# Performance work log

Measured on AMD Instinct MI355X. Metric: run time of the kernel, lower is better.

The kernel has to match this reference:

```python
import jax, jax.numpy as jnp
import numpy as np

N_NODES = 100000
N_EDGES = 1600000
IN_CH = 128          # 127 node features + 1 node_attr
HIDDEN = 2           # hidd_FV_size
OUT_CH = 128
ATTR = 6


def setup_inputs() -> dict:
    key = jax.random.key(0)
    ks = jax.random.split(key, 8)
    x = jax.random.normal(ks[0], (N_NODES, IN_CH - 1), dtype=jnp.float32)
    node_attr = jax.random.normal(ks[1], (N_NODES, 1), dtype=jnp.float32)
    edge_index = jax.random.randint(ks[2], (2, N_EDGES), 0, N_NODES, dtype=jnp.int64)
    edge_attr = jax.random.normal(ks[3], (N_EDGES, ATTR), dtype=jnp.float32)
    # lin_in: Linear(ATTR, HIDDEN * IN_CH); lin_out: Linear(HIDDEN * IN_CH, OUT_CH)
    W_in = jax.random.normal(ks[4], (ATTR, HIDDEN * IN_CH), dtype=jnp.float32) / np.sqrt(ATTR)
    b_in = jax.random.normal(ks[5], (HIDDEN * IN_CH,), dtype=jnp.float32) * 0.01
    W_out = jax.random.normal(ks[6], (HIDDEN * IN_CH, OUT_CH), dtype=jnp.float32) / np.sqrt(HIDDEN * IN_CH)
    b_out = jax.random.normal(ks[7], (OUT_CH,), dtype=jnp.float32) * 0.01
    return {"x": x, "node_attr": node_attr, "edge_index": edge_index,
            "edge_attr": edge_attr, "W_in": W_in, "b_in": b_in,
            "W_out": W_out, "b_out": b_out}


def reference(x, node_attr, edge_index, edge_attr, W_in, b_in, W_out, b_out):
    # forward: x = cat(x, node_attr) -> propagate(aggr='add') -> update
    xc = jnp.concatenate([x, node_attr], axis=1)                # [N, IN_CH]
    src, dst = edge_index[0], edge_index[1]                     # PyG: message from x_j=src, aggregated at dst
    x_j = xc[src]                                               # [E, IN_CH] gather
    # message: scaling = relu(lin_in(edge_attr)); result = scaling.reshape(E,C,H) * x_j[...,None]
    scaling = jax.nn.relu(edge_attr @ W_in + b_in)              # [E, C*H]
    msg = (scaling.reshape(-1, IN_CH, HIDDEN) * x_j[:, :, None]).reshape(-1, IN_CH * HIDDEN)
    # aggregate: scatter-add over destination nodes
    aggr = jax.ops.segment_sum(msg, dst, num_segments=N_NODES)  # [N, C*H]
    # update: lin_out -> tanh (dropout p=0 / eval mode)
    return jnp.tanh(aggr @ W_out + b_out)                       # [N, OUT_CH]
```

## Files before the change

### kernel.cpp

```cpp
#include <hip/hip_runtime.h>


#define ATTR 6
#define SCAN_CHUNK 1024


__global__ __launch_bounds__(256) void concat_kernel(
    const float* __restrict__ x, const float* __restrict__ na,
    float* __restrict__ xc, int N)
{
  const int gid = blockIdx.x * 256 + threadIdx.x;
  const int row = gid >> 5;
  const int c4 = (gid & 31) * 4;
  if (row >= N) return;
  const float* xr = x + (size_t)row * 127;
  float4 v;
  v.x = xr[c4];
  v.y = xr[c4 + 1];
  v.z = xr[c4 + 2];
  v.w = (c4 == 124) ? na[row] : xr[c4 + 3];
  *(float4*)(xc + (size_t)row * 128 + c4) = v;
}


__global__ __launch_bounds__(256) void hist_kernel(
    const int* __restrict__ ei, int* __restrict__ counts, int E)
{
  int e = blockIdx.x * 256 + threadIdx.x;
  if (e < E) atomicAdd(&counts[ei[E + e]], 1);
}

__global__ __launch_bounds__(256) void scan1_kernel(
    const int* __restrict__ counts, int* __restrict__ offsets,
    int* __restrict__ bsum, int N)
{
  __shared__ int sdata[256];
  const int t = threadIdx.x;
  const int base = blockIdx.x * SCAN_CHUNK + t * 4;
  int c[4]; int s = 0;
#pragma unroll
  for (int j = 0; j < 4; ++j) { int i = base + j; c[j] = (i < N) ? counts[i] : 0; s += c[j]; }
  sdata[t] = s;
  __syncthreads();
  for (int d = 1; d < 256; d <<= 1) {
    int tv = (t >= d) ? sdata[t - d] : 0;
    __syncthreads();
    sdata[t] += tv;
    __syncthreads();
  }
  int excl = sdata[t] - s;
#pragma unroll
  for (int j = 0; j < 4; ++j) { int i = base + j; if (i < N) offsets[i] = excl; excl += c[j]; }
  if (t == 255) bsum[blockIdx.x] = sdata[255];
}

__global__ __launch_bounds__(256) void scan2_kernel(int* __restrict__ bsum, int nb)
{
  __shared__ int sdata[256];
  const int t = threadIdx.x;
  int v = (t < nb) ? bsum[t] : 0;
  int orig = v;
  sdata[t] = v;
  __syncthreads();
  for (int d = 1; d < 256; d <<= 1) {
    int tv = (t >= d) ? sdata[t - d] : 0;
    __syncthreads();
    sdata[t] += tv;
    __syncthreads();
  }
  if (t < nb) bsum[t] = sdata[t] - orig;
}

__global__ __launch_bounds__(256) void scan3_kernel(
    int* __restrict__ offsets, int* __restrict__ cursors,
    const int* __restrict__ bsum, int N, int E)
{
  const int base = blockIdx.x * SCAN_CHUNK + threadIdx.x * 4;
  const int add = bsum[blockIdx.x];
#pragma unroll
  for (int j = 0; j < 4; ++j) {
    int i = base + j;
    if (i < N) { int v = offsets[i] + add; offsets[i] = v; cursors[i] = v; }
  }
  if (blockIdx.x == 0 && threadIdx.x == 0) offsets[N] = E;
}

__global__ __launch_bounds__(256) void scatter_payload_kernel(
    const int* __restrict__ ei, const float* __restrict__ ea,
    int* __restrict__ cursors,
    int* __restrict__ srcs, float* __restrict__ eas, int E)
{
  int e = blockIdx.x * 256 + threadIdx.x;
  if (e < E) {
    const int dst = ei[E + e];
    const int slot = atomicAdd(&cursors[dst], 1);
    srcs[slot] = ei[e];
    const float2 a0 = *(const float2*)(ea + (size_t)e * ATTR + 0);
    const float2 a1 = *(const float2*)(ea + (size_t)e * ATTR + 2);
    const float2 a2 = *(const float2*)(ea + (size_t)e * ATTR + 4);
    float* ep = eas + (size_t)slot * ATTR;
    *(float2*)(ep + 0) = a0;
    *(float2*)(ep + 2) = a1;
    *(float2*)(ep + 4) = a2;
  }
}

__global__ __launch_bounds__(256) void scatter_kernel(
    const int* __restrict__ ei, int* __restrict__ cursors,
    int* __restrict__ perm, int* __restrict__ srcs, int E)
{
  int e = blockIdx.x * 256 + threadIdx.x;
  if (e < E) {
    int dst = ei[E + e];
    int slot = atomicAdd(&cursors[dst], 1);
    perm[slot] = e;
    srcs[slot] = ei[e];
  }
}


__global__ __launch_bounds__(256) void aggregate8_kernel(
    const float* __restrict__ xc,
    const float* __restrict__ W_in, const float* __restrict__ b_in,
    const int* __restrict__ offsets, const int* __restrict__ srcs,
    const float* __restrict__ eas,
    float* __restrict__ aggr, int N)
{
  const int L = threadIdx.x & 63;
  const int n = __builtin_amdgcn_readfirstlane(blockIdx.x * 4 + (threadIdx.x >> 6));
  if (n >= N) return;

  float2 wlo[ATTR], whi[ATTR];
#pragma unroll
  for (int a = 0; a < ATTR; ++a) {
    wlo[a] = *(const float2*)(W_in + a * 256 + 2 * L);
    whi[a] = *(const float2*)(W_in + a * 256 + 128 + 2 * L);
  }
  const float2 blo = *(const float2*)(b_in + 2 * L);
  const float2 bhi = *(const float2*)(b_in + 128 + 2 * L);

  float alo0 = 0.f, alo1 = 0.f, ahi0 = 0.f, ahi1 = 0.f;
  const int beg = offsets[n], end = offsets[n + 1];

  for (int i0 = beg; i0 < end; i0 += 8) {
    const int cnt = end - i0;
    int s8[8];
#pragma unroll
    for (int j = 0; j < 8; ++j) {
      const int idx = i0 + ((j < cnt) ? j : cnt - 1);
      s8[j] = srcs[idx];
    }
    float eav[8][ATTR];
#pragma unroll
    for (int j = 0; j < 8; ++j) {
      const int idx = i0 + ((j < cnt) ? j : cnt - 1);
#pragma unroll
      for (int a = 0; a < ATTR; ++a) eav[j][a] = eas[(size_t)idx * ATTR + a];
    }

    float xlo[8], xhi[8];
#pragma unroll
    for (int j = 0; j < 8; ++j) {
      const float* xr = xc + (size_t)s8[j] * 128;
      xlo[j] = xr[L];
      xhi[j] = xr[64 + L];
    }
#pragma unroll
    for (int j = 0; j < 8; ++j)
      if (j >= cnt) { xlo[j] = 0.f; xhi[j] = 0.f; }

#pragma unroll
    for (int j = 0; j < 8; ++j) {
      float sl0 = blo.x, sl1 = blo.y, sh0 = bhi.x, sh1 = bhi.y;
#pragma unroll
      for (int a = 0; a < ATTR; ++a) {
        sl0 = fmaf(eav[j][a], wlo[a].x, sl0);
        sl1 = fmaf(eav[j][a], wlo[a].y, sl1);
        sh0 = fmaf(eav[j][a], whi[a].x, sh0);
        sh1 = fmaf(eav[j][a], whi[a].y, sh1);
      }
      sl0 = fmaxf(sl0, 0.f); sl1 = fmaxf(sl1, 0.f);
      sh0 = fmaxf(sh0, 0.f); sh1 = fmaxf(sh1, 0.f);
      alo0 = fmaf(sl0, xlo[j], alo0);
      alo1 = fmaf(sl1, xlo[j], alo1);
      ahi0 = fmaf(sh0, xhi[j], ahi0);
      ahi1 = fmaf(sh1, xhi[j], ahi1);
    }
  }

  *(float2*)(aggr + (size_t)n * 256 + 2 * L)       = make_float2(alo0, alo1);
  *(float2*)(aggr + (size_t)n * 256 + 128 + 2 * L) = make_float2(ahi0, ahi1);
}


__global__ __launch_bounds__(256) void aggregate4_kernel(
    const float* __restrict__ x, const float* __restrict__ node_attr,
    const int* __restrict__ ei, const float* __restrict__ ea,
    const float* __restrict__ W_in, const float* __restrict__ b_in,
    const int* __restrict__ offsets, const int* __restrict__ perm,
    const int* __restrict__ srcs,
    float* __restrict__ aggr, int N)
{
  const int L = threadIdx.x & 63;
  const int n = __builtin_amdgcn_readfirstlane(blockIdx.x * 4 + (threadIdx.x >> 6));
  if (n >= N) return;

  float2 wlo[ATTR], whi[ATTR];
#pragma unroll
  for (int a = 0; a < ATTR; ++a) {
    wlo[a] = *(const float2*)(W_in + a * 256 + 2 * L);
    whi[a] = *(const float2*)(W_in + a * 256 + 128 + 2 * L);
  }
  const float2 blo = *(const float2*)(b_in + 2 * L);
  const float2 bhi = *(const float2*)(b_in + 128 + 2 * L);

  float alo0 = 0.f, alo1 = 0.f, ahi0 = 0.f, ahi1 = 0.f;
  const int beg = offsets[n], end = offsets[n + 1];

  for (int i0 = beg; i0 < end; i0 += 4) {
    const int cnt = end - i0;
    int e4[4], s4[4];
#pragma unroll
    for (int j = 0; j < 4; ++j) {
      const int idx = i0 + ((j < cnt) ? j : cnt - 1);
      e4[j] = perm[idx];
      s4[j] = srcs[idx];
    }

    float eav[4][ATTR];
#pragma unroll
    for (int j = 0; j < 4; ++j)
#pragma unroll
      for (int a = 0; a < ATTR; ++a) eav[j][a] = ea[(size_t)e4[j] * ATTR + a];

    float xlo[4], xhi[4];
#pragma unroll
    for (int j = 0; j < 4; ++j) {
      const float* xr = x + (size_t)s4[j] * 127;
      xlo[j] = xr[L];
      xhi[j] = (L == 63) ? node_attr[s4[j]] : xr[64 + L];
    }
#pragma unroll
    for (int j = 0; j < 4; ++j)
      if (j >= cnt) { xlo[j] = 0.f; xhi[j] = 0.f; }

#pragma unroll
    for (int j = 0; j < 4; ++j) {
      float sl0 = blo.x, sl1 = blo.y, sh0 = bhi.x, sh1 = bhi.y;
#pragma unroll
      for (int a = 0; a < ATTR; ++a) {
        sl0 = fmaf(eav[j][a], wlo[a].x, sl0);
        sl1 = fmaf(eav[j][a], wlo[a].y, sl1);
        sh0 = fmaf(eav[j][a], whi[a].x, sh0);
        sh1 = fmaf(eav[j][a], whi[a].y, sh1);
      }
      sl0 = fmaxf(sl0, 0.f); sl1 = fmaxf(sl1, 0.f);
      sh0 = fmaxf(sh0, 0.f); sh1 = fmaxf(sh1, 0.f);
      alo0 = fmaf(sl0, xlo[j], alo0);
      alo1 = fmaf(sl1, xlo[j], alo1);
      ahi0 = fmaf(sh0, xhi[j], ahi0);
      ahi1 = fmaf(sh1, xhi[j], ahi1);
    }
  }

  *(float2*)(aggr + (size_t)n * 256 + 2 * L)       = make_float2(alo0, alo1);
  *(float2*)(aggr + (size_t)n * 256 + 128 + 2 * L) = make_float2(ahi0, ahi1);
}


__global__ __launch_bounds__(256) void edge_kernel(
    const float* __restrict__ x, const float* __restrict__ node_attr,
    const int* __restrict__ ei, const float* __restrict__ ea,
    const float* __restrict__ W_in, const float* __restrict__ b_in,
    float* __restrict__ aggr, int E, int N, int epw)
{
  const int lane = threadIdx.x & 63;
  const int wave = blockIdx.x * (blockDim.x >> 6) + (threadIdx.x >> 6);
  const int k0 = lane << 2;
  const int c0 = lane << 1;

  float w[ATTR][4];
#pragma unroll
  for (int a = 0; a < ATTR; ++a) {
    const float4 t = *(const float4*)(W_in + a * 256 + k0);
    w[a][0] = t.x; w[a][1] = t.y; w[a][2] = t.z; w[a][3] = t.w;
  }
  const float4 bt = *(const float4*)(b_in + k0);

  const long e0 = (long)wave * epw;
  for (int i = 0; i < epw; ++i) {
    const long e = e0 + i;
    if (e >= E) return;
    const int src = ei[e];
    const int dst = ei[E + e];

    float eav[ATTR];
#pragma unroll
    for (int a = 0; a < ATTR; ++a) eav[a] = ea[(size_t)e * ATTR + a];

    float s0 = bt.x, s1 = bt.y, s2 = bt.z, s3 = bt.w;
#pragma unroll
    for (int a = 0; a < ATTR; ++a) {
      s0 = fmaf(eav[a], w[a][0], s0);
      s1 = fmaf(eav[a], w[a][1], s1);
      s2 = fmaf(eav[a], w[a][2], s2);
      s3 = fmaf(eav[a], w[a][3], s3);
    }
    s0 = fmaxf(s0, 0.f); s1 = fmaxf(s1, 0.f);
    s2 = fmaxf(s2, 0.f); s3 = fmaxf(s3, 0.f);

    const float* xr = x + (size_t)src * 127;
    const float x0 = xr[c0];
    const float x1 = (lane == 63) ? node_attr[src] : xr[c0 + 1];

    float* ap = aggr + (size_t)dst * 256 + k0;
    atomicAdd(ap + 0, s0 * x0);
    atomicAdd(ap + 1, s1 * x0);
    atomicAdd(ap + 2, s2 * x1);
    atomicAdd(ap + 3, s3 * x1);
  }
}


__global__ __launch_bounds__(256) void node_kernel2(
    const float* __restrict__ aggr, const float* __restrict__ W_out,
    const float* __restrict__ b_out, float* __restrict__ out, int N)
{
  __shared__ float Wl[64 * 128];
  __shared__ float Al[64][68];
  const int t = threadIdx.x;
  const int o4 = (t & 31) * 4;
  const int ng = t >> 5;
  const int nbase = blockIdx.x * 64;

  float acc[8][4];
#pragma unroll
  for (int j = 0; j < 8; ++j)
#pragma unroll
    for (int q = 0; q < 4; ++q) acc[j][q] = 0.f;

  for (int kc = 0; kc < 4; ++kc) {
    __syncthreads();
    const float4* wsrc = (const float4*)(W_out + kc * 64 * 128);
    float4* wdst = (float4*)Wl;
#pragma unroll
    for (int i = 0; i < 8; ++i) wdst[t + 256 * i] = wsrc[t + 256 * i];
    {
      const int r = t >> 2, q = t & 3;
      int row = nbase + r; if (row >= N) row = N - 1;
      const float4* asrc = (const float4*)(aggr + (size_t)row * 256 + kc * 64 + q * 16);
      float4 v0 = asrc[0], v1 = asrc[1], v2 = asrc[2], v3 = asrc[3];
      float4* adst = (float4*)&Al[r][q * 16];
      adst[0] = v0; adst[1] = v1; adst[2] = v2; adst[3] = v3;
    }
    __syncthreads();

    for (int k = 0; k < 64; k += 4) {
      float4 a4[8];
#pragma unroll
      for (int j = 0; j < 8; ++j) a4[j] = *(const float4*)&Al[ng * 8 + j][k];
#pragma unroll
      for (int kk = 0; kk < 4; ++kk) {
        const float4 w4 = *(const float4*)&Wl[(k + kk) * 128 + o4];
#pragma unroll
        for (int j = 0; j < 8; ++j) {
          const float av = (&a4[j].x)[kk];
          acc[j][0] = fmaf(av, w4.x, acc[j][0]);
          acc[j][1] = fmaf(av, w4.y, acc[j][1]);
          acc[j][2] = fmaf(av, w4.z, acc[j][2]);
          acc[j][3] = fmaf(av, w4.w, acc[j][3]);
        }
      }
    }
  }

  const float4 b4 = *(const float4*)(b_out + o4);
#pragma unroll
  for (int j = 0; j < 8; ++j) {
    const int n = nbase + ng * 8 + j;
    if (n < N) {
      float4 r;
      r.x = tanhf(acc[j][0] + b4.x);
      r.y = tanhf(acc[j][1] + b4.y);
      r.z = tanhf(acc[j][2] + b4.z);
      r.w = tanhf(acc[j][3] + b4.w);
      *(float4*)(out + (size_t)n * 128 + o4) = r;
    }
  }
}


extern "C" void kernel_launch(void* const* d_in, const int* in_sizes, int n_in,
                              void* d_out, int out_size, void* d_ws, size_t ws_size,
                              hipStream_t stream) {
  const float* x         = (const float*)d_in[0];
  const float* node_attr = (const float*)d_in[1];
  const int*   ei        = (const int*)d_in[2];
  const float* ea        = (const float*)d_in[3];
  const float* W_in      = (const float*)d_in[4];
  const float* b_in      = (const float*)d_in[5];
  const float* W_out     = (const float*)d_in[6];
  const float* b_out     = (const float*)d_in[7];
  float* out = (float*)d_out;

  const int N = in_sizes[0] / 127;
  const int E = in_sizes[2] / 2;

  auto align16 = [](size_t v) { return (v + 15) & ~(size_t)15; };
  const size_t szCounts  = align16((size_t)N * 4);
  const size_t szOffsets = align16(((size_t)N + 1) * 4);
  const size_t szCursors = align16((size_t)N * 4);
  const size_t szBsum    = 1024;
  const size_t szPerm    = align16((size_t)E * 4);
  const size_t szSrcs    = align16((size_t)E * 4);
  const size_t szEas     = align16((size_t)E * ATTR * 4);
  const size_t szXc      = align16((size_t)N * 128 * 4);
  const size_t szAggr    = (size_t)N * 256 * 4;

  const size_t needA = szCounts + szOffsets + szCursors + szBsum +
                       szSrcs + szEas + szXc + szAggr;
  const size_t needB = szCounts + szOffsets + szCursors + szBsum +
                       szPerm + szSrcs + szAggr;

  const int nodeBlocks = (N + 63) / 64;
  const int eb = (E + 255) / 256;
  const int nb = (N + SCAN_CHUNK - 1) / SCAN_CHUNK;

  if (ws_size >= needA) {
    char* p = (char*)d_ws;
    int* counts   = (int*)p;     p += szCounts;
    int* offsets  = (int*)p;     p += szOffsets;
    int* cursors  = (int*)p;     p += szCursors;
    int* bsum     = (int*)p;     p += szBsum;
    int* srcs     = (int*)p;     p += szSrcs;
    float* eas    = (float*)p;   p += szEas;
    float* xc     = (float*)p;   p += szXc;
    float* aggr   = (float*)p;

    hipMemsetAsync(counts, 0, (size_t)N * 4, stream);

    concat_kernel<<<(N * 32 + 255) / 256, 256, 0, stream>>>(x, node_attr, xc, N);
    hist_kernel<<<eb, 256, 0, stream>>>(ei, counts, E);
    scan1_kernel<<<nb, 256, 0, stream>>>(counts, offsets, bsum, N);
    scan2_kernel<<<1, 256, 0, stream>>>(bsum, nb);
    scan3_kernel<<<nb, 256, 0, stream>>>(offsets, cursors, bsum, N, E);
    scatter_payload_kernel<<<eb, 256, 0, stream>>>(ei, ea, cursors, srcs, eas, E);
    aggregate8_kernel<<<(N + 3) / 4, 256, 0, stream>>>(
        xc, W_in, b_in, offsets, srcs, eas, aggr, N);
    node_kernel2<<<nodeBlocks, 256, 0, stream>>>(aggr, W_out, b_out, out, N);
  } else if (ws_size >= needB) {
    char* p = (char*)d_ws;
    int* counts   = (int*)p;     p += szCounts;
    int* offsets  = (int*)p;     p += szOffsets;
    int* cursors  = (int*)p;     p += szCursors;
    int* bsum     = (int*)p;     p += szBsum;
    int* perm     = (int*)p;     p += szPerm;
    int* srcs     = (int*)p;     p += szSrcs;
    float* aggr   = (float*)p;

    hipMemsetAsync(counts, 0, (size_t)N * 4, stream);

    hist_kernel<<<eb, 256, 0, stream>>>(ei, counts, E);
    scan1_kernel<<<nb, 256, 0, stream>>>(counts, offsets, bsum, N);
    scan2_kernel<<<1, 256, 0, stream>>>(bsum, nb);
    scan3_kernel<<<nb, 256, 0, stream>>>(offsets, cursors, bsum, N, E);
    scatter_kernel<<<eb, 256, 0, stream>>>(ei, cursors, perm, srcs, E);
    aggregate4_kernel<<<(N + 3) / 4, 256, 0, stream>>>(
        x, node_attr, ei, ea, W_in, b_in, offsets, perm, srcs, aggr, N);
    node_kernel2<<<nodeBlocks, 256, 0, stream>>>(aggr, W_out, b_out, out, N);
  } else {
    float* aggr = (float*)d_ws;
    hipMemsetAsync(aggr, 0, (size_t)N * 256 * 4, stream);
    const int EPW = 4;
    const int waves = (E + EPW - 1) / EPW;
    edge_kernel<<<(waves + 3) / 4, 256, 0, stream>>>(
        x, node_attr, ei, ea, W_in, b_in, aggr, E, N, EPW);
    node_kernel2<<<nodeBlocks, 256, 0, stream>>>(aggr, W_out, b_out, out, N);
  }
}
```

Before: 569.6 us.

## Fuse histogram with last-block scan, merge scatter with concat, add tail-free aggregation

The histogram and the three-stage prefix scan become one kernel, in which the last block to finish (found through an atomic done counter) scans all counts serially in tiles. The concat work now runs as extra blocks inside the scatter kernel. The aggregate kernel handles full 8-edge chunks first, then one 4-edge chunk and single edges, which removes the clamped-index and masking work. This cuts several kernel launches and the stalls between them, but the whole scan of 100k counts now runs in a single block.

```diff
diff --git a/kernel.cpp b/kernel.cpp
--- a/kernel.cpp
+++ b/kernel.cpp
@@ -2,124 +2,115 @@
 
 
 #define ATTR 6
-#define SCAN_CHUNK 1024
-
-
-__global__ __launch_bounds__(256) void concat_kernel(
+
+
+__global__ __launch_bounds__(256) void hist_scan_kernel(
+    const int* __restrict__ ei, int* __restrict__ counts, int* __restrict__ done,
+    int* __restrict__ offsets, int* __restrict__ cursors, int E, int N)
+{
+  const int t = threadIdx.x;
+  const int e0 = blockIdx.x * 1024 + t * 4;
+  if (((E & 3) == 0) && (e0 + 4 <= E)) {
+    const int4 d = *(const int4*)(ei + E + e0);
+    atomicAdd(&counts[d.x], 1);
+    atomicAdd(&counts[d.y], 1);
+    atomicAdd(&counts[d.z], 1);
+    atomicAdd(&counts[d.w], 1);
+  } else {
+#pragma unroll
+    for (int j = 0; j < 4; ++j) {
+      const int e = e0 + j;
+      if (e < E) atomicAdd(&counts[ei[E + e]], 1);
+    }
+  }
+
+  __threadfence();
+  __syncthreads();
+  __shared__ int lastFlag;
+  if (t == 0) lastFlag = (atomicAdd(done, 1) == (int)gridDim.x - 1) ? 1 : 0;
+  __syncthreads();
+  if (!lastFlag) return;
+  __threadfence();
+
+  const int lane = t & 63;
+  const int w = t >> 6;
+  __shared__ int wsum[4];
+  int rbase = 0;
+  const int ntiles = (N + 4095) >> 12;
+  for (int tile = 0; tile < ntiles; ++tile) {
+    const int i0 = (tile << 12) + t * 16;
+    int c[16]; int s = 0;
+#pragma unroll
+    for (int j = 0; j < 16; ++j) {
+      const int i = i0 + j;
+      c[j] = (i < N) ? __hip_atomic_load(&counts[i], __ATOMIC_RELAXED,
+                                         __HIP_MEMORY_SCOPE_AGENT) : 0;
+      s += c[j];
+    }
+    int sc = s;
+#pragma unroll
+    for (int d = 1; d < 64; d <<= 1) {
+      const int u = __shfl_up(sc, d, 64);
+      if (lane >= d) sc += u;
+    }
+    if (lane == 63) wsum[w] = sc;
+    __syncthreads();
+    int wpre = 0;
+#pragma unroll
+    for (int k = 0; k < 4; ++k) if (k < w) wpre += wsum[k];
+    const int tot = wsum[0] + wsum[1] + wsum[2] + wsum[3];
+    int excl = rbase + wpre + (sc - s);
+#pragma unroll
+    for (int j = 0; j < 16; ++j) {
+      const int i = i0 + j;
+      if (i < N) { offsets[i] = excl; cursors[i] = excl; }
+      excl += c[j];
+    }
+    rbase += tot;
+    __syncthreads();
+  }
+  if (t == 0) offsets[N] = E;
+}
+
+
+__global__ __launch_bounds__(256) void scatter_concat_kernel(
+    const int* __restrict__ ei, const float* __restrict__ ea,
+    int* __restrict__ cursors, int* __restrict__ srcs, float* __restrict__ eas,
     const float* __restrict__ x, const float* __restrict__ na,
-    float* __restrict__ xc, int N)
-{
-  const int gid = blockIdx.x * 256 + threadIdx.x;
-  const int row = gid >> 5;
-  const int c4 = (gid & 31) * 4;
-  if (row >= N) return;
-  const float* xr = x + (size_t)row * 127;
-  float4 v;
-  v.x = xr[c4];
-  v.y = xr[c4 + 1];
-  v.z = xr[c4 + 2];
-  v.w = (c4 == 124) ? na[row] : xr[c4 + 3];
-  *(float4*)(xc + (size_t)row * 128 + c4) = v;
-}
-
-
-__global__ __launch_bounds__(256) void hist_kernel(
-    const int* __restrict__ ei, int* __restrict__ counts, int E)
-{
-  int e = blockIdx.x * 256 + threadIdx.x;
-  if (e < E) atomicAdd(&counts[ei[E + e]], 1);
-}
-
-__global__ __launch_bounds__(256) void scan1_kernel(
-    const int* __restrict__ counts, int* __restrict__ offsets,
-    int* __restrict__ bsum, int N)
-{
-  __shared__ int sdata[256];
-  const int t = threadIdx.x;
-  const int base = blockIdx.x * SCAN_CHUNK + t * 4;
-  int c[4]; int s = 0;
-#pragma unroll
-  for (int j = 0; j < 4; ++j) { int i = base + j; c[j] = (i < N) ? counts[i] : 0; s += c[j]; }
-  sdata[t] = s;
-  __syncthreads();
-  for (int d = 1; d < 256; d <<= 1) {
-    int tv = (t >= d) ? sdata[t - d] : 0;
-    __syncthreads();
-    sdata[t] += tv;
-    __syncthreads();
-  }
-  int excl = sdata[t] - s;
-#pragma unroll
-  for (int j = 0; j < 4; ++j) { int i = base + j; if (i < N) offsets[i] = excl; excl += c[j]; }
-  if (t == 255) bsum[blockIdx.x] = sdata[255];
-}
-
-__global__ __launch_bounds__(256) void scan2_kernel(int* __restrict__ bsum, int nb)
-{
-  __shared__ int sdata[256];
-  const int t = threadIdx.x;
-  int v = (t < nb) ? bsum[t] : 0;
-  int orig = v;
-  sdata[t] = v;
-  __syncthreads();
-  for (int d = 1; d < 256; d <<= 1) {
-    int tv = (t >= d) ? sdata[t - d] : 0;
-    __syncthreads();
-    sdata[t] += tv;
-    __syncthreads();
-  }
-  if (t < nb) bsum[t] = sdata[t] - orig;
-}
-
-__global__ __launch_bounds__(256) void scan3_kernel(
-    int* __restrict__ offsets, int* __restrict__ cursors,
-    const int* __restrict__ bsum, int N, int E)
-{
-  const int base = blockIdx.x * SCAN_CHUNK + threadIdx.x * 4;
-  const int add = bsum[blockIdx.x];
-#pragma unroll
-  for (int j = 0; j < 4; ++j) {
-    int i = base + j;
-    if (i < N) { int v = offsets[i] + add; offsets[i] = v; cursors[i] = v; }
-  }
-  if (blockIdx.x == 0 && threadIdx.x == 0) offsets[N] = E;
-}
-
-__global__ __launch_bounds__(256) void scatter_payload_kernel(
-    const int* __restrict__ ei, const float* __restrict__ ea,
-    int* __restrict__ cursors,
-    int* __restrict__ srcs, float* __restrict__ eas, int E)
-{
-  int e = blockIdx.x * 256 + threadIdx.x;
-  if (e < E) {
-    const int dst = ei[E + e];
-    const int slot = atomicAdd(&cursors[dst], 1);
-    srcs[slot] = ei[e];
-    const float2 a0 = *(const float2*)(ea + (size_t)e * ATTR + 0);
-    const float2 a1 = *(const float2*)(ea + (size_t)e * ATTR + 2);
-    const float2 a2 = *(const float2*)(ea + (size_t)e * ATTR + 4);
-    float* ep = eas + (size_t)slot * ATTR;
-    *(float2*)(ep + 0) = a0;
-    *(float2*)(ep + 2) = a1;
-    *(float2*)(ep + 4) = a2;
-  }
-}
-
-__global__ __launch_bounds__(256) void scatter_kernel(
-    const int* __restrict__ ei, int* __restrict__ cursors,
-    int* __restrict__ perm, int* __restrict__ srcs, int E)
-{
-  int e = blockIdx.x * 256 + threadIdx.x;
-  if (e < E) {
-    int dst = ei[E + e];
-    int slot = atomicAdd(&cursors[dst], 1);
-    perm[slot] = e;
-    srcs[slot] = ei[e];
-  }
-}
-
-
-__global__ __launch_bounds__(256) void aggregate8_kernel(
+    float* __restrict__ xc, int E, int N, int SB)
+{
+  if ((int)blockIdx.x < SB) {
+    const int e = blockIdx.x * 256 + threadIdx.x;
+    if (e < E) {
+      const int dst = ei[E + e];
+      const int slot = atomicAdd(&cursors[dst], 1);
+      srcs[slot] = ei[e];
+      const float2 a0 = *(const float2*)(ea + (size_t)e * ATTR + 0);
+      const float2 a1 = *(const float2*)(ea + (size_t)e * ATTR + 2);
+      const float2 a2 = *(const float2*)(ea + (size_t)e * ATTR + 4);
+      float* ep = eas + (size_t)slot * ATTR;
+      *(float2*)(ep + 0) = a0;
+      *(float2*)(ep + 2) = a1;
+      *(float2*)(ep + 4) = a2;
+    }
+  } else {
+    const int gid = (blockIdx.x - SB) * 256 + threadIdx.x;
+    const int row = gid >> 5;
+    const int c4 = (gid & 31) * 4;
+    if (row < N) {
+      const float* xr = x + (size_t)row * 127;
+      float4 v;
+      v.x = xr[c4];
+      v.y = xr[c4 + 1];
+      v.z = xr[c4 + 2];
+      v.w = (c4 == 124) ? na[row] : xr[c4 + 3];
+      *(float4*)(xc + (size_t)row * 128 + c4) = v;
+    }
+  }
+}
+
+
+__global__ __launch_bounds__(256) void aggregate8b_kernel(
     const float* __restrict__ xc,
     const float* __restrict__ W_in, const float* __restrict__ b_in,
     const int* __restrict__ offsets, const int* __restrict__ srcs,
@@ -140,23 +131,19 @@
   const float2 bhi = *(const float2*)(b_in + 128 + 2 * L);
 
   float alo0 = 0.f, alo1 = 0.f, ahi0 = 0.f, ahi1 = 0.f;
-  const int beg = offsets[n], end = offsets[n + 1];
-
-  for (int i0 = beg; i0 < end; i0 += 8) {
-    const int cnt = end - i0;
+  const int beg = __builtin_amdgcn_readfirstlane(offsets[n]);
+  const int end = __builtin_amdgcn_readfirstlane(offsets[n + 1]);
+
+  int i0 = beg;
+  for (; i0 + 8 <= end; i0 += 8) {
     int s8[8];
 #pragma unroll
-    for (int j = 0; j < 8; ++j) {
-      const int idx = i0 + ((j < cnt) ? j : cnt - 1);
-      s8[j] = srcs[idx];
-    }
+    for (int j = 0; j < 8; ++j) s8[j] = srcs[i0 + j];
     float eav[8][ATTR];
 #pragma unroll
-    for (int j = 0; j < 8; ++j) {
-      const int idx = i0 + ((j < cnt) ? j : cnt - 1);
-#pragma unroll
-      for (int a = 0; a < ATTR; ++a) eav[j][a] = eas[(size_t)idx * ATTR + a];
-    }
+    for (int j = 0; j < 8; ++j)
+#pragma unroll
+      for (int a = 0; a < ATTR; ++a) eav[j][a] = eas[(size_t)(i0 + j) * ATTR + a];
 
     float xlo[8], xhi[8];
 #pragma unroll
@@ -165,10 +152,6 @@
       xlo[j] = xr[L];
       xhi[j] = xr[64 + L];
     }
-#pragma unroll
-    for (int j = 0; j < 8; ++j)
-      if (j >= cnt) { xlo[j] = 0.f; xhi[j] = 0.f; }
-
 #pragma unroll
     for (int j = 0; j < 8; ++j) {
       float sl0 = blo.x, sl1 = blo.y, sh0 = bhi.x, sh1 = bhi.y;
@@ -187,63 +170,22 @@
       ahi1 = fmaf(sh1, xhi[j], ahi1);
     }
   }
-
-  *(float2*)(aggr + (size_t)n * 256 + 2 * L)       = make_float2(alo0, alo1);
-  *(float2*)(aggr + (size_t)n * 256 + 128 + 2 * L) = make_float2(ahi0, ahi1);
-}
-
-
-__global__ __launch_bounds__(256) void aggregate4_kernel(
-    const float* __restrict__ x, const float* __restrict__ node_attr,
-    const int* __restrict__ ei, const float* __restrict__ ea,
-    const float* __restrict__ W_in, const float* __restrict__ b_in,
-    const int* __restrict__ offsets, const int* __restrict__ perm,
-    const int* __restrict__ srcs,
-    float* __restrict__ aggr, int N)
-{
-  const int L = threadIdx.x & 63;
-  const int n = __builtin_amdgcn_readfirstlane(blockIdx.x * 4 + (threadIdx.x >> 6));
-  if (n >= N) return;
-
-  float2 wlo[ATTR], whi[ATTR];
-#pragma unroll
-  for (int a = 0; a < ATTR; ++a) {
-    wlo[a] = *(const float2*)(W_in + a * 256 + 2 * L);
-    whi[a] = *(const float2*)(W_in + a * 256 + 128 + 2 * L);
-  }
-  const float2 blo = *(const float2*)(b_in + 2 * L);
-  const float2 bhi = *(const float2*)(b_in + 128 + 2 * L);
-
-  float alo0 = 0.f, alo1 = 0.f, ahi0 = 0.f, ahi1 = 0.f;
-  const int beg = offsets[n], end = offsets[n + 1];
-
-  for (int i0 = beg; i0 < end; i0 += 4) {
-    const int cnt = end - i0;
-    int e4[4], s4[4];
+  if (i0 + 4 <= end) {
+    int s4[4];
+#pragma unroll
+    for (int j = 0; j < 4; ++j) s4[j] = srcs[i0 + j];
+    float eav[4][ATTR];
+#pragma unroll
+    for (int j = 0; j < 4; ++j)
+#pragma unroll
+      for (int a = 0; a < ATTR; ++a) eav[j][a] = eas[(size_t)(i0 + j) * ATTR + a];
+    float xlo[4], xhi[4];
 #pragma unroll
     for (int j = 0; j < 4; ++j) {
-      const int idx = i0 + ((j < cnt) ? j : cnt - 1);
-      e4[j] = perm[idx];
-      s4[j] = srcs[idx];
-    }
-
-    float eav[4][ATTR];
-#pragma unroll
-    for (int j = 0; j < 4; ++j)
-#pragma unroll
-      for (int a = 0; a < ATTR; ++a) eav[j][a] = ea[(size_t)e4[j] * ATTR + a];
-
-    float xlo[4], xhi[4];
-#pragma unroll
-    for (int j = 0; j < 4; ++j) {
-      const float* xr = x + (size_t)s4[j] * 127;
+      const float* xr = xc + (size_t)s4[j] * 128;
       xlo[j] = xr[L];
-      xhi[j] = (L == 63) ? node_attr[s4[j]] : xr[64 + L];
-    }
-#pragma unroll
-    for (int j = 0; j < 4; ++j)
-      if (j >= cnt) { xlo[j] = 0.f; xhi[j] = 0.f; }
-
+      xhi[j] = xr[64 + L];
+    }
 #pragma unroll
     for (int j = 0; j < 4; ++j) {
       float sl0 = blo.x, sl1 = blo.y, sh0 = bhi.x, sh1 = bhi.y;
@@ -261,6 +203,115 @@
       ahi0 = fmaf(sh0, xhi[j], ahi0);
       ahi1 = fmaf(sh1, xhi[j], ahi1);
     }
+    i0 += 4;
+  }
+  for (; i0 < end; ++i0) {
+    const int s = srcs[i0];
+    float eav[ATTR];
+#pragma unroll
+    for (int a = 0; a < ATTR; ++a) eav[a] = eas[(size_t)i0 * ATTR + a];
+    const float* xr = xc + (size_t)s * 128;
+    const float xl = xr[L];
+    const float xh = xr[64 + L];
+    float sl0 = blo.x, sl1 = blo.y, sh0 = bhi.x, sh1 = bhi.y;
+#pragma unroll
+    for (int a = 0; a < ATTR; ++a) {
+      sl0 = fmaf(eav[a], wlo[a].x, sl0);
+      sl1 = fmaf(eav[a], wlo[a].y, sl1);
+      sh0 = fmaf(eav[a], whi[a].x, sh0);
+      sh1 = fmaf(eav[a], whi[a].y, sh1);
+    }
+    sl0 = fmaxf(sl0, 0.f); sl1 = fmaxf(sl1, 0.f);
+    sh0 = fmaxf(sh0, 0.f); sh1 = fmaxf(sh1, 0.f);
+    alo0 = fmaf(sl0, xl, alo0);
+    alo1 = fmaf(sl1, xl, alo1);
+    ahi0 = fmaf(sh0, xh, ahi0);
+    ahi1 = fmaf(sh1, xh, ahi1);
+  }
+
+  *(float2*)(aggr + (size_t)n * 256 + 2 * L)       = make_float2(alo0, alo1);
+  *(float2*)(aggr + (size_t)n * 256 + 128 + 2 * L) = make_float2(ahi0, ahi1);
+}
+
+
+__global__ __launch_bounds__(256) void scatter_kernel(
+    const int* __restrict__ ei, int* __restrict__ cursors,
+    int* __restrict__ perm, int* __restrict__ srcs, int E)
+{
+  int e = blockIdx.x * 256 + threadIdx.x;
+  if (e < E) {
+    int dst = ei[E + e];
+    int slot = atomicAdd(&cursors[dst], 1);
+    perm[slot] = e;
+    srcs[slot] = ei[e];
+  }
+}
+
+__global__ __launch_bounds__(256) void aggregate4_kernel(
+    const float* __restrict__ x, const float* __restrict__ node_attr,
+    const int* __restrict__ ei, const float* __restrict__ ea,
+    const float* __restrict__ W_in, const float* __restrict__ b_in,
+    const int* __restrict__ offsets, const int* __restrict__ perm,
+    const int* __restrict__ srcs,
+    float* __restrict__ aggr, int N)
+{
+  const int L = threadIdx.x & 63;
+  const int n = __builtin_amdgcn_readfirstlane(blockIdx.x * 4 + (threadIdx.x >> 6));
+  if (n >= N) return;
+
+  float2 wlo[ATTR], whi[ATTR];
+#pragma unroll
+  for (int a = 0; a < ATTR; ++a) {
+    wlo[a] = *(const float2*)(W_in + a * 256 + 2 * L);
+    whi[a] = *(const float2*)(W_in + a * 256 + 128 + 2 * L);
+  }
+  const float2 blo = *(const float2*)(b_in + 2 * L);
+  const float2 bhi = *(const float2*)(b_in + 128 + 2 * L);
+
+  float alo0 = 0.f, alo1 = 0.f, ahi0 = 0.f, ahi1 = 0.f;
+  const int beg = offsets[n], end = offsets[n + 1];
+
+  for (int i0 = beg; i0 < end; i0 += 4) {
+    const int cnt = end - i0;
+    int e4[4], s4[4];
+#pragma unroll
+    for (int j = 0; j < 4; ++j) {
+      const int idx = i0 + ((j < cnt) ? j : cnt - 1);
+      e4[j] = perm[idx];
+      s4[j] = srcs[idx];
+    }
+    float eav[4][ATTR];
+#pragma unroll
+    for (int j = 0; j < 4; ++j)
+#pragma unroll
+      for (int a = 0; a < ATTR; ++a) eav[j][a] = ea[(size_t)e4[j] * ATTR + a];
+    float xlo[4], xhi[4];
+#pragma unroll
+    for (int j = 0; j < 4; ++j) {
+      const float* xr = x + (size_t)s4[j] * 127;
+      xlo[j] = xr[L];
+      xhi[j] = (L == 63) ? node_attr[s4[j]] : xr[64 + L];
+    }
+#pragma unroll
+    for (int j = 0; j < 4; ++j)
+      if (j >= cnt) { xlo[j] = 0.f; xhi[j] = 0.f; }
+#pragma unroll
+    for (int j = 0; j < 4; ++j) {
+      float sl0 = blo.x, sl1 = blo.y, sh0 = bhi.x, sh1 = bhi.y;
+#pragma unroll
+      for (int a = 0; a < ATTR; ++a) {
+        sl0 = fmaf(eav[j][a], wlo[a].x, sl0);
+        sl1 = fmaf(eav[j][a], wlo[a].y, sl1);
+        sh0 = fmaf(eav[j][a], whi[a].x, sh0);
+        sh1 = fmaf(eav[j][a], whi[a].y, sh1);
+      }
+      sl0 = fmaxf(sl0, 0.f); sl1 = fmaxf(sl1, 0.f);
+      sh0 = fmaxf(sh0, 0.f); sh1 = fmaxf(sh1, 0.f);
+      alo0 = fmaf(sl0, xlo[j], alo0);
+      alo1 = fmaf(sl1, xlo[j], alo1);
+      ahi0 = fmaf(sh0, xhi[j], ahi0);
+      ahi1 = fmaf(sh1, xhi[j], ahi1);
+    }
   }
 
   *(float2*)(aggr + (size_t)n * 256 + 2 * L)       = make_float2(alo0, alo1);
@@ -408,63 +459,58 @@
 
   auto align16 = [](size_t v) { return (v + 15) & ~(size_t)15; };
   const size_t szCounts  = align16((size_t)N * 4);
+  const size_t szDone    = 16;
   const size_t szOffsets = align16(((size_t)N + 1) * 4);
   const size_t szCursors = align16((size_t)N * 4);
-  const size_t szBsum    = 1024;
   const size_t szPerm    = align16((size_t)E * 4);
   const size_t szSrcs    = align16((size_t)E * 4);
   const size_t szEas     = align16((size_t)E * ATTR * 4);
   const size_t szXc      = align16((size_t)N * 128 * 4);
   const size_t szAggr    = (size_t)N * 256 * 4;
 
-  const size_t needA = szCounts + szOffsets + szCursors + szBsum +
+  const size_t needA = szCounts + szDone + szOffsets + szCursors +
                        szSrcs + szEas + szXc + szAggr;
-  const size_t needB = szCounts + szOffsets + szCursors + szBsum +
+  const size_t needB = szCounts + szDone + szOffsets + szCursors +
                        szPerm + szSrcs + szAggr;
 
   const int nodeBlocks = (N + 63) / 64;
-  const int eb = (E + 255) / 256;
-  const int nb = (N + SCAN_CHUNK - 1) / SCAN_CHUNK;
+  const int histBlocks = (E + 1023) / 1024;
+  const int SB = (E + 255) / 256;
+  const int CB = (N * 32 + 255) / 256;
 
   if (ws_size >= needA) {
     char* p = (char*)d_ws;
     int* counts   = (int*)p;     p += szCounts;
+    int* done     = (int*)p;     p += szDone;
     int* offsets  = (int*)p;     p += szOffsets;
     int* cursors  = (int*)p;     p += szCursors;
-    int* bsum     = (int*)p;     p += szBsum;
     int* srcs     = (int*)p;     p += szSrcs;
     float* eas    = (float*)p;   p += szEas;
     float* xc     = (float*)p;   p += szXc;
     float* aggr   = (float*)p;
 
-    hipMemsetAsync(counts, 0, (size_t)N * 4, stream);
-
-    concat_kernel<<<(N * 32 + 255) / 256, 256, 0, stream>>>(x, node_attr, xc, N);
-    hist_kernel<<<eb, 256, 0, stream>>>(ei, counts, E);
-    scan1_kernel<<<nb, 256, 0, stream>>>(counts, offsets, bsum, N);
-    scan2_kernel<<<1, 256, 0, stream>>>(bsum, nb);
-    scan3_kernel<<<nb, 256, 0, stream>>>(offsets, cursors, bsum, N, E);
-    scatter_payload_kernel<<<eb, 256, 0, stream>>>(ei, ea, cursors, srcs, eas, E);
-    aggregate8_kernel<<<(N + 3) / 4, 256, 0, stream>>>(
+    hipMemsetAsync(counts, 0, szCounts + szDone, stream);
+    hist_scan_kernel<<<histBlocks, 256, 0, stream>>>(
+        ei, counts, done, offsets, cursors, E, N);
+    scatter_concat_kernel<<<SB + CB, 256, 0, stream>>>(
+        ei, ea, cursors, srcs, eas, x, node_attr, xc, E, N, SB);
+    aggregate8b_kernel<<<(N + 3) / 4, 256, 0, stream>>>(
         xc, W_in, b_in, offsets, srcs, eas, aggr, N);
     node_kernel2<<<nodeBlocks, 256, 0, stream>>>(aggr, W_out, b_out, out, N);
   } else if (ws_size >= needB) {
     char* p = (char*)d_ws;
     int* counts   = (int*)p;     p += szCounts;
+    int* done     = (int*)p;     p += szDone;
     int* offsets  = (int*)p;     p += szOffsets;
     int* cursors  = (int*)p;     p += szCursors;
-    int* bsum     = (int*)p;     p += szBsum;
     int* perm     = (int*)p;     p += szPerm;
     int* srcs     = (int*)p;     p += szSrcs;
     float* aggr   = (float*)p;
 
-    hipMemsetAsync(counts, 0, (size_t)N * 4, stream);
-
-    hist_kernel<<<eb, 256, 0, stream>>>(ei, counts, E);
-    scan1_kernel<<<nb, 256, 0, stream>>>(counts, offsets, bsum, N);
-    scan2_kernel<<<1, 256, 0, stream>>>(bsum, nb);
-    scan3_kernel<<<nb, 256, 0, stream>>>(offsets, cursors, bsum, N, E);
-    scatter_kernel<<<eb, 256, 0, stream>>>(ei, cursors, perm, srcs, E);
+    hipMemsetAsync(counts, 0, szCounts + szDone, stream);
+    hist_scan_kernel<<<histBlocks, 256, 0, stream>>>(
+        ei, counts, done, offsets, cursors, E, N);
+    scatter_kernel<<<SB, 256, 0, stream>>>(ei, cursors, perm, srcs, E);
     aggregate4_kernel<<<(N + 3) / 4, 256, 0, stream>>>(
         x, node_attr, ei, ea, W_in, b_in, offsets, perm, srcs, aggr, N);
     node_kernel2<<<nodeBlocks, 256, 0, stream>>>(aggr, W_out, b_out, out, N);
```

Measured after the change: 751.2 us. +31.9%, slower.
